# Performance work log

Hardware: AMD Instinct MI355X
Metric: run time of the kernel (lower is better)

## Reference

```python
import jax, jax.numpy as jnp
import numpy as np

N_EMBD = 1024
N_HEAD = 16
LATENT = 64
HEAD_DIM = N_EMBD // N_HEAD
B, T = 2, 2048
SCALE = 1.0 / np.sqrt(LATENT)


def setup_inputs() -> dict:
    key = jax.random.key(0)
    ks = jax.random.split(key, 10)
    s = lambda fan_in: 1.0 / np.sqrt(fan_in)
    return {
        "x": jax.random.normal(ks[0], (B, T, N_EMBD), dtype=jnp.float32),
        "Wq": jax.random.normal(ks[1], (N_EMBD, N_EMBD), dtype=jnp.float32) * s(N_EMBD),
        "bq": jnp.zeros((N_EMBD,), dtype=jnp.float32),
        "Wk": jax.random.normal(ks[2], (N_EMBD, N_HEAD * LATENT), dtype=jnp.float32) * s(N_EMBD),
        "bk": jnp.zeros((N_HEAD * LATENT,), dtype=jnp.float32),
        "Wv": jax.random.normal(ks[3], (N_EMBD, N_HEAD * LATENT), dtype=jnp.float32) * s(N_EMBD),
        "bv": jnp.zeros((N_HEAD * LATENT,), dtype=jnp.float32),
        "Wo": jax.random.normal(ks[4], (N_HEAD * LATENT, N_EMBD), dtype=jnp.float32) * s(N_HEAD * LATENT),
        "bo": jnp.zeros((N_EMBD,), dtype=jnp.float32),
        "Wc": jax.random.normal(ks[5], (HEAD_DIM, LATENT), dtype=jnp.float32) * s(HEAD_DIM),
    }


def reference(x, Wq, bq, Wk, bk, Wv, bv, Wo, bo, Wc):
    Bv, Tv, C = x.shape
    # projections
    q = (x @ Wq + bq).reshape(Bv, Tv, N_HEAD, HEAD_DIM)        # [B,T,H,Dh]
    k = (x @ Wk + bk).reshape(Bv, Tv, N_HEAD, LATENT)          # [B,T,H,L]
    v = (x @ Wv + bv).reshape(Bv, Tv, N_HEAD, LATENT)          # [B,T,H,L]
    # compress q into latent dim: [B,T,H,L]
    qc = jnp.einsum("bthd,dl->bthl", q, Wc)
    # attention scores [B,H,T,T]
    att = jnp.einsum("bthl,bshl->bhts", qc, k) * SCALE
    causal = jnp.tril(jnp.ones((Tv, Tv), dtype=bool))
    att = jnp.where(causal[None, None], att, -jnp.inf)
    att = jax.nn.softmax(att, axis=-1)
    y = jnp.einsum("bhts,bshl->bthl", att, v).reshape(Bv, Tv, N_HEAD * LATENT)
    return y @ Wo + bo
```

## Files before the change

### kernel.cpp

```cpp
#include <hip/hip_runtime.h>
#include <stdint.h>

#define TT 2048
#define BB 2
#define MROWS (BB*TT)
#define LSCALE 0.18033688011112043f

typedef unsigned short u16;
typedef __bf16 bf16x8 __attribute__((ext_vector_type(8)));
typedef float f32x4 __attribute__((ext_vector_type(4)));
typedef short s16x8 __attribute__((ext_vector_type(8)));
typedef unsigned short u16x4 __attribute__((ext_vector_type(4)));

#define GLOBAL_AS const __attribute__((address_space(1))) void*
#define LDS_AS __attribute__((address_space(3))) void*

__device__ __forceinline__ u16 f2b(float f){
  uint32_t u = __builtin_bit_cast(uint32_t, f);
  u = (u + 0x7FFFu + ((u >> 16) & 1u)) >> 16;
  return (u16)u;
}
__device__ __forceinline__ float b2f(u16 u){
  return __builtin_bit_cast(float, (uint32_t)u << 16);
}

__global__ void cvt_bf16(const float* __restrict__ in, u16* __restrict__ out, int n4){
  int i = blockIdx.x * 256 + threadIdx.x;
  if (i < n4){
    float4 v = ((const float4*)in)[i];
    u16x4 o; o.x = f2b(v.x); o.y = f2b(v.y); o.z = f2b(v.z); o.w = f2b(v.w);
    ((u16x4*)out)[i] = o;
  }
}

__global__ __launch_bounds__(256) void build_wqc(const float* __restrict__ Wq,
                                                 const float* __restrict__ Wc,
                                                 const float* __restrict__ bq,
                                                 float* __restrict__ Wqc,
                                                 float* __restrict__ bqc){
  __shared__ float wc[4096];
  const int t = threadIdx.x;
  #pragma unroll
  for (int i = 0; i < 16; ++i) wc[i * 256 + t] = Wc[i * 256 + t];
  __syncthreads();
  if (blockIdx.x == 256){
    #pragma unroll
    for (int i = 0; i < 4; ++i){
      int nn = t * 4 + i;
      int h = nn >> 6, lc = nn & 63;
      float acc = 0.f;
      #pragma unroll
      for (int dd = 0; dd < 64; ++dd) acc += bq[h * 64 + dd] * wc[dd * 64 + lc];
      bqc[nn] = acc;
    }
    return;
  }
  const int idx = blockIdx.x * 256 + t;
  const int d = idx >> 6;
  const int h = (idx >> 2) & 15;
  const int lq = idx & 3;
  float wqr[64];
  const float4* wq4 = (const float4*)(Wq + (size_t)d * 1024 + h * 64);
  #pragma unroll
  for (int i = 0; i < 16; ++i){
    float4 v = wq4[i];
    wqr[i * 4 + 0] = v.x; wqr[i * 4 + 1] = v.y; wqr[i * 4 + 2] = v.z; wqr[i * 4 + 3] = v.w;
  }
  float* outp = Wqc + (size_t)d * 1024 + h * 64 + lq * 16;
  #pragma unroll
  for (int j = 0; j < 16; ++j){
    int lc = lq * 16 + j;
    float acc = 0.f;
    #pragma unroll
    for (int dd = 0; dd < 64; ++dd) acc += wqr[dd] * wc[dd * 64 + lc];
    outp[j] = acc;
  }
}

__global__ void transpose_w4(const float* __restrict__ s0, const float* __restrict__ s1,
                             const float* __restrict__ s2, const float* __restrict__ s3,
                             u16* __restrict__ o0, u16* __restrict__ o1,
                             u16* __restrict__ o2, u16* __restrict__ o3){
  const int z = blockIdx.z;
  const float* in = (z == 0) ? s0 : (z == 1) ? s1 : (z == 2) ? s2 : s3;
  u16* out = (z == 0) ? o0 : (z == 1) ? o1 : (z == 2) ? o2 : o3;
  __shared__ float t[32][33];
  int tx = threadIdx.x & 31, ty = threadIdx.x >> 5;
  int c0 = blockIdx.x * 32, r0 = blockIdx.y * 32;
  #pragma unroll
  for (int i = 0; i < 32; i += 8)
    t[ty + i][tx] = in[(size_t)(r0 + ty + i) * 1024 + c0 + tx];
  __syncthreads();
  #pragma unroll
  for (int i = 0; i < 32; i += 8)
    out[(size_t)(c0 + ty + i) * 1024 + r0 + tx] = f2b(t[tx][ty + i]);
}

__global__ void transpose_v(const u16* __restrict__ vb, u16* __restrict__ vt){
  __shared__ u16 t[32][34];
  int tx = threadIdx.x & 31, ty = threadIdx.x >> 5;
  int s0 = blockIdx.x * 32, d0 = blockIdx.y * 32, bh = blockIdx.z;
  int b = bh >> 4, h = bh & 15;
  #pragma unroll
  for (int i = 0; i < 32; i += 8)
    t[ty + i][tx] = vb[(size_t)(b * TT + s0 + ty + i) * 1024 + h * 64 + d0 + tx];
  __syncthreads();
  #pragma unroll
  for (int i = 0; i < 32; i += 8)
    vt[((size_t)bh * 64 + d0 + ty + i) * TT + s0 + tx] = t[tx][ty + i];
}

__device__ __forceinline__ void gemm_tile(const u16* __restrict__ A, const u16* __restrict__ BT,
                                          int m0, int n0, int K, f32x4 (&acc)[4][4],
                                          u16* As, u16* Bs, int tid){
  const int wv = tid >> 6, l = tid & 63;
  const int aoff = ((wv >> 1) * 64 + (l & 15)) * 32 + ((l >> 4) << 3);
  const int boff = ((wv & 1) * 64 + (l & 15)) * 32 + ((l >> 4) << 3);
  const int ob0 = wv * 1024 + l * 16;
  for (int kt = 0; kt < K; kt += 32){
    __syncthreads();
    #pragma unroll
    for (int j = 0; j < 2; ++j){
      int ob = ob0 + j * 4096;
      int row = ob >> 6, col = (ob & 63) >> 1;
      __builtin_amdgcn_global_load_lds((GLOBAL_AS)(A + (size_t)(m0 + row) * 1024 + kt + col),
                                       (LDS_AS)(As + wv * 512 + j * 2048), 16, 0, 0);
      __builtin_amdgcn_global_load_lds((GLOBAL_AS)(BT + (size_t)(n0 + row) * 1024 + kt + col),
                                       (LDS_AS)(Bs + wv * 512 + j * 2048), 16, 0, 0);
    }
    __syncthreads();
    bf16x8 av[4], bw[4];
    #pragma unroll
    for (int m = 0; m < 4; ++m) av[m] = *(const bf16x8*)(As + aoff + m * 512);
    #pragma unroll
    for (int n = 0; n < 4; ++n) bw[n] = *(const bf16x8*)(Bs + boff + n * 512);
    #pragma unroll
    for (int m = 0; m < 4; ++m)
      #pragma unroll
      for (int n = 0; n < 4; ++n)
        acc[m][n] = __builtin_amdgcn_mfma_f32_16x16x32_bf16(av[m], bw[n], acc[m][n], 0, 0, 0);
  }
}

__global__ __launch_bounds__(256) void gemm_qkv(
    const u16* __restrict__ xb,
    const u16* __restrict__ W0T, const u16* __restrict__ W1T, const u16* __restrict__ W2T,
    const float* __restrict__ b0, const float* __restrict__ b1, const float* __restrict__ b2,
    u16* __restrict__ o0, u16* __restrict__ o1, u16* __restrict__ o2){
  __shared__ u16 As[4096], Bs[4096];
  const int z = blockIdx.z;
  const u16* BT = (z == 0) ? W0T : (z == 1) ? W1T : W2T;
  const float* bias = (z == 0) ? b0 : (z == 1) ? b1 : b2;
  u16* Out = (z == 0) ? o0 : (z == 1) ? o1 : o2;
  const float osc = (z == 0) ? LSCALE : 1.0f;
  const int n0 = blockIdx.x * 128, m0 = blockIdx.y * 128;
  const int tid = threadIdx.x, wv = tid >> 6, l = tid & 63;
  f32x4 acc[4][4] = {};
  gemm_tile(xb, BT, m0, n0, 1024, acc, As, Bs, tid);
  const int wr = wv >> 1, wc = wv & 1;
  #pragma unroll
  for (int n = 0; n < 4; ++n){
    int col = n0 + wc * 64 + n * 16 + (l & 15);
    float bb = bias[col];
    #pragma unroll
    for (int m = 0; m < 4; ++m){
      int r0 = m0 + wr * 64 + m * 16 + ((l >> 4) << 2);
      #pragma unroll
      for (int r = 0; r < 4; ++r)
        Out[(size_t)(r0 + r) * 1024 + col] = f2b((acc[m][n][r] + bb) * osc);
    }
  }
}

__global__ __launch_bounds__(256) void gemm_fp32out(
    const u16* __restrict__ A, const u16* __restrict__ BT,
    const float* __restrict__ bias, float* __restrict__ Out){
  __shared__ u16 As[4096], Bs[4096];
  const int n0 = blockIdx.x * 128, m0 = blockIdx.y * 128;
  const int tid = threadIdx.x, wv = tid >> 6, l = tid & 63;
  f32x4 acc[4][4] = {};
  gemm_tile(A, BT, m0, n0, 1024, acc, As, Bs, tid);
  const int wr = wv >> 1, wc = wv & 1;
  #pragma unroll
  for (int n = 0; n < 4; ++n){
    int col = n0 + wc * 64 + n * 16 + (l & 15);
    float bb = bias[col];
    #pragma unroll
    for (int m = 0; m < 4; ++m){
      int r0 = m0 + wr * 64 + m * 16 + ((l >> 4) << 2);
      #pragma unroll
      for (int r = 0; r < 4; ++r)
        Out[(size_t)(r0 + r) * 1024 + col] = acc[m][n][r] + bb;
    }
  }
}

__device__ const uint8_t gtab[48] = {
  31, 95, 30, 143,  94, 29, 93, 28, 142,  92, 27, 91, 26, 141,
  90, 25, 89, 24, 140,  88, 23, 87, 22, 139,  86, 21, 85, 20, 138,
  84, 19, 83, 18, 137,  82, 17, 81, 16, 136,  80, 135, 134, 133, 132,
  131, 130, 129, 128
};

__global__ __launch_bounds__(256) void attn(
    const u16* __restrict__ qcg, const u16* __restrict__ kg,
    const u16* __restrict__ vtg, u16* __restrict__ yg,
    u16* __restrict__ yp, float* __restrict__ mp, float* __restrict__ lp){
  __shared__ u16 Ks[2][4096], Vs[2][4096];
  __shared__ u16 Ps[4096];
  const int idx = blockIdx.x;
  const int g = idx >> 5, bh = idx & 31;
  const int gv_ = gtab[g];
  const int qt = gv_ & 31, piece = gv_ >> 6;
  const int hh = (qt + 2) >> 1;
  const int st0 = (piece == 1) ? hh : 0;
  const int st1 = (piece == 0) ? hh : qt + 1;
  const int pid = (piece == 2) ? -1 : ((31 - qt) * 32 + bh) * 2 + piece;
  const int b = bh >> 4, h = bh & 15;
  const int q0 = qt * 64;
  const int tid = threadIdx.x, wv = tid >> 6, l = tid & 63;
  const int c4 = l >> 4, q16 = l & 15;
  const size_t base = (size_t)b * TT * 1024 + h * 64;
  const u16* Q = qcg + base;
  const u16* K = kg + base;
  const u16* Vt = vtg + (size_t)bh * 64 * TT;

  const int sr = tid >> 3;
  const int sc = (tid & 7) ^ (sr & 7);
  const u16* gK = K + (size_t)sr * 1024 + sc * 8;
  const u16* gV = Vt + (size_t)sr * TT + sc * 8;

  {
    const size_t o = (size_t)st0 * 64;
    u16* kd = &Ks[0][0] + wv * 512;
    u16* vd = &Vs[0][0] + wv * 512;
    __builtin_amdgcn_global_load_lds((GLOBAL_AS)(gK + o * 1024), (LDS_AS)kd, 16, 0, 0);
    __builtin_amdgcn_global_load_lds((GLOBAL_AS)(gK + (o + 32) * 1024), (LDS_AS)(kd + 2048), 16, 0, 0);
    __builtin_amdgcn_global_load_lds((GLOBAL_AS)(gV + o), (LDS_AS)vd, 16, 0, 0);
    __builtin_amdgcn_global_load_lds((GLOBAL_AS)(gV + o + 32 * TT), (LDS_AS)(vd + 2048), 16, 0, 0);
  }

  bf16x8 qf[2];
  {
    int qr = q0 + wv * 16 + q16;
    #pragma unroll
    for (int ks = 0; ks < 2; ++ks)
      qf[ks] = *(const bf16x8*)(Q + (size_t)qr * 1024 + ks * 32 + (c4 << 3));
  }
  f32x4 yacc[4] = {};
  float mrow = -1e30f, srow = 0.f;

  uint32_t* const PsW = (uint32_t*)Ps + wv * 512 + q16 * 32;
  const int pm = (q16 & 7) << 2;

  for (int st = st0; st < st1; ++st){
    const int cur = (st - st0) & 1;
    const u16* Kc = &Ks[cur][0];
    const u16* Vc = &Vs[cur][0];
    if (st + 1 < st1){
      const size_t o = (size_t)(st + 1) * 64;
      u16* kd = &Ks[cur ^ 1][0] + wv * 512;
      u16* vd = &Vs[cur ^ 1][0] + wv * 512;
      __builtin_amdgcn_global_load_lds((GLOBAL_AS)(gK + o * 1024), (LDS_AS)kd, 16, 0, 0);
      __builtin_amdgcn_global_load_lds((GLOBAL_AS)(gK + (o + 32) * 1024), (LDS_AS)(kd + 2048), 16, 0, 0);
      __builtin_amdgcn_global_load_lds((GLOBAL_AS)(gV + o), (LDS_AS)vd, 16, 0, 0);
      __builtin_amdgcn_global_load_lds((GLOBAL_AS)(gV + o + 32 * TT), (LDS_AS)(vd + 2048), 16, 0, 0);
      asm volatile("s_waitcnt vmcnt(4)" ::: "memory");
    } else {
      asm volatile("s_waitcnt vmcnt(0)" ::: "memory");
    }
    __builtin_amdgcn_sched_barrier(0);
    __builtin_amdgcn_s_barrier();
    __builtin_amdgcn_sched_barrier(0);
    const int s0 = st * 64;
    f32x4 sf[4] = {};
    __builtin_amdgcn_s_setprio(1);
    #pragma unroll
    for (int ks = 0; ks < 2; ++ks)
      #pragma unroll
      for (int nf = 0; nf < 4; ++nf){
        int r = nf * 16 + q16, c = ks * 4 + c4;
        bf16x8 kf = *(const bf16x8*)(Kc + (r * 8 + (c ^ (r & 7))) * 8);
        sf[nf] = __builtin_amdgcn_mfma_f32_16x16x32_bf16(kf, qf[ks], sf[nf], 0, 0, 0);
      }
    __builtin_amdgcn_s_setprio(0);
    const int qa = q0 + wv * 16 + q16;
    float p[4][4];
    const bool domask = (st == qt);
    #pragma unroll
    for (int nf = 0; nf < 4; ++nf)
      #pragma unroll
      for (int r = 0; r < 4; ++r){
        float v_ = sf[nf][r];
        if (domask && (s0 + nf * 16 + c4 * 4 + r > qa)) v_ = -1e30f;
        p[nf][r] = v_;
      }
    float tmax = p[0][0];
    #pragma unroll
    for (int nf = 0; nf < 4; ++nf)
      #pragma unroll
      for (int r = 0; r < 4; ++r) tmax = fmaxf(tmax, p[nf][r]);
    tmax = fmaxf(tmax, __shfl_xor(tmax, 16));
    tmax = fmaxf(tmax, __shfl_xor(tmax, 32));
    if (__any(tmax > mrow + 8.0f)){
      float mnew = fmaxf(mrow, tmax);
      float resc = exp2f(mrow - mnew);
      srow *= resc;
      mrow = mnew;
      float rq[4];
      #pragma unroll
      for (int r = 0; r < 4; ++r) rq[r] = __shfl(resc, (l & 48) | (c4 * 4 + r));
      #pragma unroll
      for (int df = 0; df < 4; ++df)
        #pragma unroll
        for (int r = 0; r < 4; ++r) yacc[df][r] *= rq[r];
    }
    float tsum = 0.f;
    #pragma unroll
    for (int nf = 0; nf < 4; ++nf)
      #pragma unroll
      for (int r = 0; r < 4; ++r){ float e = exp2f(p[nf][r] - mrow); p[nf][r] = e; tsum += e; }
    tsum += __shfl_xor(tsum, 16);
    tsum += __shfl_xor(tsum, 32);
    srow += tsum;
    #pragma unroll
    for (int nf = 0; nf < 4; ++nf){
      uint32_t w0, w1;
      asm volatile("v_cvt_pk_bf16_f32 %0, %1, %2" : "=v"(w0) : "v"(p[nf][0]), "v"(p[nf][1]));
      asm volatile("v_cvt_pk_bf16_f32 %0, %1, %2" : "=v"(w1) : "v"(p[nf][2]), "v"(p[nf][3]));
      *(uint64_t*)(PsW + ((nf * 8 + c4 * 2) ^ pm)) = (uint64_t)w0 | ((uint64_t)w1 << 32);
    }
    asm volatile("s_waitcnt lgkmcnt(0)" ::: "memory");
    __builtin_amdgcn_sched_barrier(0);
    __builtin_amdgcn_s_setprio(1);
    #pragma unroll
    for (int ks2 = 0; ks2 < 2; ++ks2){
      bf16x8 pf = *(const bf16x8*)(PsW + ((ks2 * 16 + c4 * 4) ^ pm));
      #pragma unroll
      for (int df = 0; df < 4; ++df){
        int rd = df * 16 + q16, cd = ks2 * 4 + c4;
        bf16x8 vf = *(const bf16x8*)(Vc + (rd * 8 + (cd ^ (rd & 7))) * 8);
        yacc[df] = __builtin_amdgcn_mfma_f32_16x16x32_bf16(pf, vf, yacc[df], 0, 0, 0);
      }
    }
    __builtin_amdgcn_s_setprio(0);
    __builtin_amdgcn_s_barrier();
  }

  if (pid >= 0){
    #pragma unroll
    for (int df = 0; df < 4; ++df){
      int d = df * 16 + q16;
      int qq = wv * 16 + c4 * 4;
      #pragma unroll
      for (int r = 0; r < 4; ++r)
        yp[(size_t)pid * 4096 + (qq + r) * 64 + d] = f2b(yacc[df][r]);
    }
    if (c4 == 0){
      mp[pid * 64 + wv * 16 + q16] = mrow;
      lp[pid * 64 + wv * 16 + q16] = srow;
    }
  } else {
    float sq[4];
    #pragma unroll
    for (int r = 0; r < 4; ++r) sq[r] = __shfl(srow, (l & 48) | (c4 * 4 + r));
    #pragma unroll
    for (int df = 0; df < 4; ++df){
      int d = df * 16 + q16;
      int qq = q0 + wv * 16 + c4 * 4;
      #pragma unroll
      for (int r = 0; r < 4; ++r){
        float val = yacc[df][r] / sq[r];
        yg[(size_t)(b * TT + qq + r) * 1024 + h * 64 + d] = f2b(val);
      }
    }
  }
}

__global__ __launch_bounds__(256) void attn_combine(
    const u16* __restrict__ yp, const float* __restrict__ mp, const float* __restrict__ lp,
    u16* __restrict__ yg){
  const int cid = blockIdx.x;
  const int qt = 31 - (cid >> 5), bh = cid & 31;
  const int pid0 = cid * 2;
  const int t = threadIdx.x;
  const int q = t >> 2, dc = (t & 3) * 16;
  float m1 = mp[pid0 * 64 + q], m2 = mp[(pid0 + 1) * 64 + q];
  float l1 = lp[pid0 * 64 + q], l2 = lp[(pid0 + 1) * 64 + q];
  float ms = fmaxf(m1, m2);
  float w1 = exp2f(m1 - ms), w2 = exp2f(m2 - ms);
  float inv = 1.f / (l1 * w1 + l2 * w2);
  w1 *= inv; w2 *= inv;
  const int b = bh >> 4, h = bh & 15;
  const s16x8* p1 = (const s16x8*)(yp + (size_t)pid0 * 4096 + q * 64 + dc);
  const s16x8* p2 = (const s16x8*)(yp + (size_t)(pid0 + 1) * 4096 + q * 64 + dc);
  u16* dst = yg + (size_t)(b * TT + qt * 64 + q) * 1024 + h * 64 + dc;
  #pragma unroll
  for (int j2 = 0; j2 < 2; ++j2){
    s16x8 a = p1[j2], c = p2[j2];
    s16x8 o;
    #pragma unroll
    for (int j = 0; j < 8; ++j)
      o[j] = (short)f2b(b2f((u16)a[j]) * w1 + b2f((u16)c[j]) * w2);
    *(s16x8*)(dst + j2 * 8) = o;
  }
}

extern "C" void kernel_launch(void* const* d_in, const int* in_sizes, int n_in,
                              void* d_out, int out_size, void* d_ws, size_t ws_size,
                              hipStream_t stream){
  (void)in_sizes; (void)n_in; (void)out_size; (void)ws_size;
  const float* x  = (const float*)d_in[0];
  const float* Wq = (const float*)d_in[1];
  const float* bq = (const float*)d_in[2];
  const float* Wk = (const float*)d_in[3];
  const float* bk = (const float*)d_in[4];
  const float* Wv = (const float*)d_in[5];
  const float* bv = (const float*)d_in[6];
  const float* Wo = (const float*)d_in[7];
  const float* bo = (const float*)d_in[8];
  const float* Wc = (const float*)d_in[9];
  float* out = (float*)d_out;

  char* wsb = (char*)d_ws;
  u16* xb    = (u16*)(wsb);
  u16* yb    = (u16*)(wsb);
  u16* qcb   = (u16*)(wsb + (8u  << 20));
  u16* kb    = (u16*)(wsb + (16u << 20));
  u16* vb    = (u16*)(wsb + (24u << 20));
  u16* yp    = (u16*)(wsb + (24u << 20));
  u16* vtb   = (u16*)(wsb + (33u << 20));
  float* Wqcf = (float*)(wsb + (33u << 20));
  float* mp  = (float*)(wsb + (41u << 20));
  float* lp  = (float*)(wsb + (41u << 20) + (1u<<19));
  u16* WqcT  = (u16*)(wsb + (42u << 20));
  u16* WkT   = (u16*)(wsb + (44u << 20));
  u16* WvT   = (u16*)(wsb + (46u << 20));
  u16* WoT   = (u16*)(wsb + (48u << 20));
  float* bqc  = (float*)(wsb + (50u << 20));

  cvt_bf16<<<4096, 256, 0, stream>>>(x, xb, MROWS * 1024 / 4);
  build_wqc<<<257, 256, 0, stream>>>(Wq, Wc, bq, Wqcf, bqc);
  transpose_w4<<<dim3(32, 32, 4), 256, 0, stream>>>(Wqcf, Wk, Wv, Wo, WqcT, WkT, WvT, WoT);
  gemm_qkv<<<dim3(8, 32, 3), 256, 0, stream>>>(xb, WqcT, WkT, WvT, bqc, bk, bv, qcb, kb, vb);
  transpose_v<<<dim3(64, 2, 32), 256, 0, stream>>>(vb, vtb);
  attn<<<dim3(1536), 256, 0, stream>>>(qcb, kb, vtb, yb, yp, mp, lp);
  attn_combine<<<dim3(512), 256, 0, stream>>>(yp, mp, lp, yb);
  gemm_fp32out<<<dim3(8, 32), 256, 0, stream>>>(yb, WoT, bo, out);
}
```

Baseline: 133.8 us.

## Transpose PV MFMA output layout and drop K/V double buffering in attention

```diff
diff --git a/kernel.cpp b/kernel.cpp
--- a/kernel.cpp
+++ b/kernel.cpp
@@ -206,7 +206,7 @@
     const u16* __restrict__ qcg, const u16* __restrict__ kg,
     const u16* __restrict__ vtg, u16* __restrict__ yg,
     u16* __restrict__ yp, float* __restrict__ mp, float* __restrict__ lp){
-  __shared__ u16 Ks[2][4096], Vs[2][4096];
+  __shared__ u16 Ks[4096], Vs[4096];
   __shared__ u16 Ps[4096];
   const int idx = blockIdx.x;
   const int g = idx >> 5, bh = idx & 31;
@@ -230,16 +230,6 @@
   const u16* gK = K + (size_t)sr * 1024 + sc * 8;
   const u16* gV = Vt + (size_t)sr * TT + sc * 8;
 
-  {
-    const size_t o = (size_t)st0 * 64;
-    u16* kd = &Ks[0][0] + wv * 512;
-    u16* vd = &Vs[0][0] + wv * 512;
-    __builtin_amdgcn_global_load_lds((GLOBAL_AS)(gK + o * 1024), (LDS_AS)kd, 16, 0, 0);
-    __builtin_amdgcn_global_load_lds((GLOBAL_AS)(gK + (o + 32) * 1024), (LDS_AS)(kd + 2048), 16, 0, 0);
-    __builtin_amdgcn_global_load_lds((GLOBAL_AS)(gV + o), (LDS_AS)vd, 16, 0, 0);
-    __builtin_amdgcn_global_load_lds((GLOBAL_AS)(gV + o + 32 * TT), (LDS_AS)(vd + 2048), 16, 0, 0);
-  }
-
   bf16x8 qf[2];
   {
     int qr = q0 + wv * 16 + q16;
@@ -253,22 +243,18 @@
   uint32_t* const PsW = (uint32_t*)Ps + wv * 512 + q16 * 32;
   const int pm = (q16 & 7) << 2;
 
+  u16* const kd = Ks + wv * 512;
+  u16* const vd = Vs + wv * 512;
+
   for (int st = st0; st < st1; ++st){
-    const int cur = (st - st0) & 1;
-    const u16* Kc = &Ks[cur][0];
-    const u16* Vc = &Vs[cur][0];
-    if (st + 1 < st1){
-      const size_t o = (size_t)(st + 1) * 64;
-      u16* kd = &Ks[cur ^ 1][0] + wv * 512;
-      u16* vd = &Vs[cur ^ 1][0] + wv * 512;
+    {
+      const size_t o = (size_t)st * 64;
       __builtin_amdgcn_global_load_lds((GLOBAL_AS)(gK + o * 1024), (LDS_AS)kd, 16, 0, 0);
       __builtin_amdgcn_global_load_lds((GLOBAL_AS)(gK + (o + 32) * 1024), (LDS_AS)(kd + 2048), 16, 0, 0);
       __builtin_amdgcn_global_load_lds((GLOBAL_AS)(gV + o), (LDS_AS)vd, 16, 0, 0);
       __builtin_amdgcn_global_load_lds((GLOBAL_AS)(gV + o + 32 * TT), (LDS_AS)(vd + 2048), 16, 0, 0);
-      asm volatile("s_waitcnt vmcnt(4)" ::: "memory");
-    } else {
-      asm volatile("s_waitcnt vmcnt(0)" ::: "memory");
-    }
+    }
+    asm volatile("s_waitcnt vmcnt(0)" ::: "memory");
     __builtin_amdgcn_sched_barrier(0);
     __builtin_amdgcn_s_barrier();
     __builtin_amdgcn_sched_barrier(0);
@@ -280,7 +266,7 @@
       #pragma unroll
       for (int nf = 0; nf < 4; ++nf){
         int r = nf * 16 + q16, c = ks * 4 + c4;
-        bf16x8 kf = *(const bf16x8*)(Kc + (r * 8 + (c ^ (r & 7))) * 8);
+        bf16x8 kf = *(const bf16x8*)(Ks + (r * 8 + (c ^ (r & 7))) * 8);
         sf[nf] = __builtin_amdgcn_mfma_f32_16x16x32_bf16(kf, qf[ks], sf[nf], 0, 0, 0);
       }
     __builtin_amdgcn_s_setprio(0);
@@ -307,13 +293,10 @@
       float resc = exp2f(mrow - mnew);
       srow *= resc;
       mrow = mnew;
-      float rq[4];
-      #pragma unroll
-      for (int r = 0; r < 4; ++r) rq[r] = __shfl(resc, (l & 48) | (c4 * 4 + r));
       #pragma unroll
       for (int df = 0; df < 4; ++df)
         #pragma unroll
-        for (int r = 0; r < 4; ++r) yacc[df][r] *= rq[r];
+        for (int r = 0; r < 4; ++r) yacc[df][r] *= resc;
     }
     float tsum = 0.f;
     #pragma unroll
@@ -339,8 +322,8 @@
       #pragma unroll
       for (int df = 0; df < 4; ++df){
         int rd = df * 16 + q16, cd = ks2 * 4 + c4;
-        bf16x8 vf = *(const bf16x8*)(Vc + (rd * 8 + (cd ^ (rd & 7))) * 8);
-        yacc[df] = __builtin_amdgcn_mfma_f32_16x16x32_bf16(pf, vf, yacc[df], 0, 0, 0);
+        bf16x8 vf = *(const bf16x8*)(Vs + (rd * 8 + (cd ^ (rd & 7))) * 8);
+        yacc[df] = __builtin_amdgcn_mfma_f32_16x16x32_bf16(vf, pf, yacc[df], 0, 0, 0);
       }
     }
     __builtin_amdgcn_s_setprio(0);
@@ -348,31 +331,27 @@
   }
 
   if (pid >= 0){
+    const int qq = wv * 16 + q16;
     #pragma unroll
     for (int df = 0; df < 4; ++df){
-      int d = df * 16 + q16;
-      int qq = wv * 16 + c4 * 4;
+      int d0 = df * 16 + c4 * 4;
       #pragma unroll
       for (int r = 0; r < 4; ++r)
-        yp[(size_t)pid * 4096 + (qq + r) * 64 + d] = f2b(yacc[df][r]);
+        yp[(size_t)pid * 4096 + qq * 64 + d0 + r] = f2b(yacc[df][r]);
     }
     if (c4 == 0){
-      mp[pid * 64 + wv * 16 + q16] = mrow;
-      lp[pid * 64 + wv * 16 + q16] = srow;
+      mp[pid * 64 + qq] = mrow;
+      lp[pid * 64 + qq] = srow;
     }
   } else {
-    float sq[4];
-    #pragma unroll
-    for (int r = 0; r < 4; ++r) sq[r] = __shfl(srow, (l & 48) | (c4 * 4 + r));
+    const float inv = 1.f / srow;
+    const int qq = q0 + wv * 16 + q16;
     #pragma unroll
     for (int df = 0; df < 4; ++df){
-      int d = df * 16 + q16;
-      int qq = q0 + wv * 16 + c4 * 4;
-      #pragma unroll
-      for (int r = 0; r < 4; ++r){
-        float val = yacc[df][r] / sq[r];
-        yg[(size_t)(b * TT + qq + r) * 1024 + h * 64 + d] = f2b(val);
-      }
+      int d0 = df * 16 + c4 * 4;
+      #pragma unroll
+      for (int r = 0; r < 4; ++r)
+        yg[(size_t)(b * TT + qq) * 1024 + h * 64 + d0 + r] = f2b(yacc[df][r] * inv);
     }
   }
 }
```

Result: no change. 132.0 us (-1.4%).
